# Kernel tuning notes

Measured on AMD Instinct MI355X. Metric: run time of the kernel, lower is better.

## Reference

```python
import math
import jax, jax.numpy as jnp
import numpy as np

B, T, C = 2, 2048, 1024
NH = 16
HS = C // NH
WIN = 256

def setup_inputs() -> dict:
    key = jax.random.key(0)
    k1, k2, k3 = jax.random.split(key, 3)
    x = jax.random.normal(k1, (B, T, C), dtype=jnp.float32)
    # Linear weights stored as (in, out) so y = x @ W
    scale_attn = 1.0 / math.sqrt(C)
    W_attn = jax.random.normal(k2, (C, 3 * C), dtype=jnp.float32) * scale_attn
    W_proj = jax.random.normal(k3, (C, C), dtype=jnp.float32) * scale_attn
    return {"x": x, "W_attn": W_attn, "W_proj": W_proj}

def reference(x, W_attn, W_proj):
    Bs, Ts, Cs = x.shape
    W = min(WIN, Ts)
    qkv = x @ W_attn                                  # [B,T,3C]
    q, k, v = jnp.split(qkv, 3, axis=-1)
    # [B,T,C] -> [B,NH,T,HS]
    q = q.reshape(Bs, Ts, NH, HS).transpose(0, 2, 1, 3)
    k = k.reshape(Bs, Ts, NH, HS).transpose(0, 2, 1, 3)
    v = v.reshape(Bs, Ts, NH, HS).transpose(0, 2, 1, 3)
    att = jnp.einsum('bhqd,bhkd->bhqk', q, k) * (1.0 / math.sqrt(HS))
    i_idx = jnp.arange(Ts)[:, None]
    j_idx = jnp.arange(Ts)[None, :]
    mask = (j_idx <= i_idx) & (i_idx - j_idx < W)      # causal sliding window
    att = jnp.where(mask[None, None, :, :], att, -jnp.inf)
    att = jax.nn.softmax(att, axis=-1)
    y = jnp.einsum('bhqk,bhkd->bhqd', att, v)          # [B,NH,T,HS]
    y = y.transpose(0, 2, 1, 3).reshape(Bs, Ts, Cs)
    return y @ W_proj
```

## Files before the change

kernel.cpp:

```cpp
#include <hip/hip_runtime.h>
#include <hip/hip_bf16.h>
#include <cstdint>

#define B_   2
#define T_   2048
#define C_   1024
#define NH_  16
#define HS_  64
#define WIN_ 256
#define M_   (B_*T_)

typedef __attribute__((ext_vector_type(8)))  short          short8;
typedef __attribute__((ext_vector_type(8)))  unsigned short ushortx8;
typedef __attribute__((ext_vector_type(8)))  __bf16         bf16x8;
typedef __attribute__((ext_vector_type(4)))  float          floatx4;
typedef __attribute__((ext_vector_type(16))) float          floatx16;

__device__ __forceinline__ unsigned short f2bf(float f) {
    union { float f; uint32_t u; } v; v.f = f;
    uint32_t r = (v.u + 0x7FFFu + ((v.u >> 16) & 1u)) >> 16;
    return (unsigned short)r;
}

__device__ __forceinline__ floatx4 mfma16(short8 a, short8 b, floatx4 c) {
    return __builtin_amdgcn_mfma_f32_16x16x32_bf16(
        __builtin_bit_cast(bf16x8, a), __builtin_bit_cast(bf16x8, b), c, 0, 0, 0);
}
__device__ __forceinline__ floatx16 mfma32(short8 a, short8 b, floatx16 c) {
    return __builtin_amdgcn_mfma_f32_32x32x16_bf16(
        __builtin_bit_cast(bf16x8, a), __builtin_bit_cast(bf16x8, b), c, 0, 0, 0);
}

__device__ __forceinline__ void async16(const void* g, void* l) {
    __builtin_amdgcn_global_load_lds(
        (const __attribute__((address_space(1))) void*)g,
        (__attribute__((address_space(3))) void*)l, 16, 0, 0);
}

#define NB_CONV 4096
#define NB_WA   768
#define NB_WP   256

__device__ void transpose_tile(const float* __restrict__ in, unsigned short* __restrict__ out,
                               int K, int N, int kt, int nt, unsigned short (*tile)[65])
{
    const int k0 = kt * 64, n0 = nt * 64;
    const int tr = threadIdx.x >> 4;
    const int tc = (threadIdx.x & 15) * 4;
    #pragma unroll
    for (int it = 0; it < 4; it++) {
        int row = tr + it * 16;
        float4 v = *(const float4*)&in[(size_t)(k0 + row) * N + n0 + tc];
        tile[row][tc + 0] = f2bf(v.x);
        tile[row][tc + 1] = f2bf(v.y);
        tile[row][tc + 2] = f2bf(v.z);
        tile[row][tc + 3] = f2bf(v.w);
    }
    __syncthreads();
    #pragma unroll
    for (int it = 0; it < 4; it++) {
        int nrow = tr + it * 16;
        ushort4 h;
        h.x = tile[tc + 0][nrow]; h.y = tile[tc + 1][nrow];
        h.z = tile[tc + 2][nrow]; h.w = tile[tc + 3][nrow];
        *(ushort4*)&out[(size_t)(n0 + nrow) * K + k0 + tc] = h;
    }
}

__global__ __launch_bounds__(256)
void prep_kernel(const float* __restrict__ x, const float* __restrict__ W_attn,
                 const float* __restrict__ W_proj,
                 unsigned short* __restrict__ xb, unsigned short* __restrict__ Wa_t,
                 unsigned short* __restrict__ Wp_t)
{
    __shared__ unsigned short tile[64][65];
    const int bid = blockIdx.x;
    if (bid < NB_CONV) {
        int i = (bid * 256 + threadIdx.x) * 4;
        float4 v = *(const float4*)&x[i];
        ushort4 h;
        h.x = f2bf(v.x); h.y = f2bf(v.y); h.z = f2bf(v.z); h.w = f2bf(v.w);
        *(ushort4*)&xb[i] = h;
    } else if (bid < NB_CONV + NB_WA) {
        int idx = bid - NB_CONV;
        transpose_tile(W_attn, Wa_t, C_, 3 * C_, idx / 48, idx % 48, tile);
    } else {
        int idx = bid - NB_CONV - NB_WA;
        transpose_tile(W_proj, Wp_t, C_, C_, idx / 16, idx % 16, tile);
    }
}

template<int MT, bool OUT_BF16, bool VSPLIT>
__global__ __launch_bounds__(256)
void gemm32(const unsigned short* __restrict__ A,
            const unsigned short* __restrict__ Bt,
            void* __restrict__ Cp, unsigned short* __restrict__ vt,
            int M, int N, int K)
{
    constexpr int BK = 64;
    constexpr int BM = 64 * MT;
    __shared__ unsigned short As[BM * BK];
    __shared__ unsigned short Bs[128 * BK];

    const int tid  = threadIdx.x;
    const int lane = tid & 63;
    const int wave = tid >> 6;
    const int l32  = lane & 31;
    const int hi   = lane >> 5;
    const int px   = l32 & 7;
    const int wm   = (wave & 1) * 32 * MT;
    const int wn   = (wave >> 1) * 64;
    const int m0   = blockIdx.y * BM;
    const int n0   = blockIdx.x * 128;

    const int ri = lane >> 3;
    const int pg = lane & 7;
    const int gg = pg ^ ri;

    floatx16 acc[MT][2];
    #pragma unroll
    for (int i = 0; i < MT; i++)
        #pragma unroll
        for (int j = 0; j < 2; j++) acc[i][j] = (floatx16)(0.f);

    const unsigned short* gA = &A[(size_t)(m0 + wave * 8 + ri) * K + gg * 8];
    const unsigned short* gB = &Bt[(size_t)(n0 + wave * 8 + ri) * K + gg * 8];
    unsigned short* lA = &As[(wave * 8) * BK];
    unsigned short* lB = &Bs[(wave * 8) * BK];

    for (int k0 = 0; k0 < K; k0 += BK) {
        #pragma unroll
        for (int s = 0; s < 2 * MT; s++)
            async16(gA + k0 + (size_t)s * 32 * K, lA + s * 32 * BK);
        #pragma unroll
        for (int s = 0; s < 4; s++)
            async16(gB + k0 + (size_t)s * 32 * K, lB + s * 32 * BK);
        __syncthreads();

        #pragma unroll
        for (int ks = 0; ks < 4; ks++) {
            short8 af[MT], bfr[2];
            #pragma unroll
            for (int i = 0; i < MT; i++) {
                int r = wm + i * 32 + l32;
                int p = (ks * 2 + hi) ^ px;
                af[i] = *(const short8*)(&As[r * BK + p * 8]);
            }
            #pragma unroll
            for (int j = 0; j < 2; j++) {
                int r = wn + j * 32 + l32;
                int p = (ks * 2 + hi) ^ px;
                bfr[j] = *(const short8*)(&Bs[r * BK + p * 8]);
            }
            #pragma unroll
            for (int i = 0; i < MT; i++)
                #pragma unroll
                for (int j = 0; j < 2; j++)
                    acc[i][j] = mfma32(af[i], bfr[j], acc[i][j]);
        }
        __syncthreads();
    }

    #pragma unroll
    for (int i = 0; i < MT; i++)
        #pragma unroll
        for (int j = 0; j < 2; j++) {
            const int col  = n0 + wn + j * 32 + l32;
            const int row0 = m0 + wm + i * 32 + 4 * hi;
            if (VSPLIT && col >= 2 * C_) {
                const int hd = col - 2 * C_;
                const int hh = hd >> 6, d = hd & 63;
                #pragma unroll
                for (int g = 0; g < 4; g++) {
                    int rowg = row0 + 8 * g;
                    int bb = rowg >> 11, t = rowg & (T_ - 1);
                    ushort4 h4;
                    h4.x = f2bf(acc[i][j][g * 4 + 0]);
                    h4.y = f2bf(acc[i][j][g * 4 + 1]);
                    h4.z = f2bf(acc[i][j][g * 4 + 2]);
                    h4.w = f2bf(acc[i][j][g * 4 + 3]);
                    *(ushort4*)&vt[((size_t)(bb * NH_ + hh) * 64 + d) * T_ + t] = h4;
                }
            } else {
                #pragma unroll
                for (int g = 0; g < 4; g++)
                    #pragma unroll
                    for (int rr = 0; rr < 4; rr++) {
                        int row = row0 + 8 * g + rr;
                        if (OUT_BF16)
                            ((unsigned short*)Cp)[(size_t)row * N + col] = f2bf(acc[i][j][g * 4 + rr]);
                        else
                            ((float*)Cp)[(size_t)row * N + col] = acc[i][j][g * 4 + rr];
                    }
            }
        }
}

__global__ __launch_bounds__(256)
void attn_kernel(const unsigned short* __restrict__ qkv,
                 const unsigned short* __restrict__ vt,
                 unsigned short* __restrict__ y)
{
    __shared__ unsigned short Ks[64 * 64];
    __shared__ unsigned short Vs[64 * 64];
    __shared__ unsigned short Ps[4][16 * 72];

    const int tid  = threadIdx.x;
    const int lane = tid & 63;
    const int wave = tid >> 6;
    const int l16  = lane & 15;
    const int quad = lane >> 4;
    const int sw   = l16 & 7;

    const int g  = blockIdx.x;
    const int yq = g >> 3;
    const int hb = (g & 7) + 8 * (yq >> 5);
    const int qt = yq & 31;
    const int h  = hb & 15;
    const int b  = hb >> 4;

    const int q0b = qt * 64;
    const int q0w = q0b + wave * 16;
    const size_t base = (size_t)b * T_;
    const int ROW  = 3 * C_;
    const int qoff = h * HS_;
    const int koff = C_ + h * HS_;
    const size_t vbase = ((size_t)(b * NH_ + h) * 64) * T_;
    unsigned short* Pstrip = Ps[wave];
    const float SC = 0.125f * 1.44269504f;

    const int ri = lane >> 3;
    const int gg = (lane & 7) ^ ri;

    short8 aq[2];
    #pragma unroll
    for (int ks = 0; ks < 2; ks++)
        aq[ks] = *(const short8*)&qkv[(base + q0w + l16) * ROW + qoff + ks * 32 + quad * 8];

    floatx4 O[4];
    #pragma unroll
    for (int j = 0; j < 4; j++) O[j] = (floatx4){0.f, 0.f, 0.f, 0.f};
    float psum[4] = {0.f, 0.f, 0.f, 0.f};

    int kb_lo = q0b - (WIN_ - 1);
    kb_lo = (kb_lo > 0 ? kb_lo : 0) & ~63;

    for (int kb = kb_lo; kb <= q0b; kb += 64) {
        __syncthreads();
        #pragma unroll
        for (int c = 0; c < 2; c++) {
            int row = wave * 16 + c * 8;
            async16(&qkv[(base + kb + row + ri) * ROW + koff + gg * 8],
                    &Ks[row * 64]);
            async16(&vt[vbase + (size_t)(row + ri) * T_ + kb + gg * 8],
                    &Vs[row * 64]);
        }
        __syncthreads();

        floatx4 s[4];
        #pragma unroll
        for (int nt = 0; nt < 4; nt++) s[nt] = (floatx4){0.f, 0.f, 0.f, 0.f};
        #pragma unroll
        for (int ks = 0; ks < 2; ks++)
            #pragma unroll
            for (int nt = 0; nt < 4; nt++) {
                short8 bk = *(const short8*)&Ks[(nt * 16 + l16) * 64
                                                + (((ks * 4 + quad) ^ sw) * 8)];
                s[nt] = mfma16(aq[ks], bk, s[nt]);
            }

        #pragma unroll
        for (int nt = 0; nt < 4; nt++)
            #pragma unroll
            for (int r = 0; r < 4; r++) {
                int dist = (q0w + quad * 4 + r) - (kb + nt * 16 + l16);
                float sv = ((unsigned)dist < (unsigned)WIN_) ? s[nt][r] * SC : -1e30f;
                float e = exp2f(sv);
                psum[r] += e;
                s[nt][r] = e;
            }

        #pragma unroll
        for (int nt = 0; nt < 4; nt++)
            #pragma unroll
            for (int r = 0; r < 4; r++)
                Pstrip[(quad * 4 + r) * 72 + nt * 16 + l16] = f2bf(s[nt][r]);

        #pragma unroll
        for (int ks = 0; ks < 2; ks++) {
            short8 ap = *(const short8*)&Pstrip[l16 * 72 + ks * 32 + quad * 8];
            #pragma unroll
            for (int jt = 0; jt < 4; jt++) {
                short8 bv = *(const short8*)&Vs[(jt * 16 + l16) * 64
                                                + (((ks * 4 + quad) ^ sw) * 8)];
                O[jt] = mfma16(ap, bv, O[jt]);
            }
        }
    }

    #pragma unroll
    for (int r = 0; r < 4; r++) {
        #pragma unroll
        for (int off = 8; off >= 1; off >>= 1)
            psum[r] += __shfl_xor(psum[r], off, 64);
    }

    #pragma unroll
    for (int jt = 0; jt < 4; jt++)
        #pragma unroll
        for (int r = 0; r < 4; r++)
            Pstrip[(quad * 4 + r) * 72 + jt * 16 + l16] = f2bf(O[jt][r] / psum[r]);
    #pragma unroll
    for (int it = 0; it < 2; it++) {
        int c = lane + 64 * it;
        int qr = c >> 3, dc = (c & 7) * 8;
        *(ushortx8*)&y[(base + q0w + qr) * C_ + qoff + dc] =
            *(const ushortx8*)&Pstrip[qr * 72 + dc];
    }
}

extern "C" void kernel_launch(void* const* d_in, const int* in_sizes, int n_in,
                              void* d_out, int out_size, void* d_ws, size_t ws_size,
                              hipStream_t stream)
{
    const float* x      = (const float*)d_in[0];
    const float* W_attn = (const float*)d_in[1];
    const float* W_proj = (const float*)d_in[2];
    float* out = (float*)d_out;

    unsigned short* xb   = (unsigned short*)d_ws;
    unsigned short* Wa_t = xb   + (size_t)M_ * C_;
    unsigned short* Wp_t = Wa_t + (size_t)3 * C_ * C_;
    unsigned short* qkv  = Wp_t + (size_t)C_ * C_;
    unsigned short* y    = qkv  + (size_t)M_ * 3 * C_;
    unsigned short* vtg  = y    + (size_t)M_ * C_;

    dim3 blk(256);
    prep_kernel<<<NB_CONV + NB_WA + NB_WP, blk, 0, stream>>>(x, W_attn, W_proj, xb, Wa_t, Wp_t);
    gemm32<2, true, true><<<dim3((3 * C_) / 128, M_ / 128), blk, 0, stream>>>(
        xb, Wa_t, qkv, vtg, M_, 3 * C_, C_);
    attn_kernel<<<(T_ / 64) * NH_ * B_, blk, 0, stream>>>(qkv, vtg, y);
    gemm32<1, false, false><<<dim3(C_ / 128, M_ / 64), blk, 0, stream>>>(
        y, Wp_t, out, nullptr, M_, C_, C_);
}
```

Measured before the change: 150.8 us.

## Use 256x256 double-buffered 512-thread GEMM tile for the QKV projection

Replaces the QKV projection GEMM with a dedicated 8-wave kernel. Each block computes a 256x256 output tile and double-buffers the A and B LDS tiles, so the next K-slice loads while the current one is multiplied. The aim is more operand reuse per global load and overlap of loads with MFMA work. The cost is about 128KB of LDS per block and only 192 blocks in the grid, which risks leaving CUs idle and capping occupancy at one block per CU. The output projection keeps a simplified fp32-output version of the old kernel.

```diff
diff --git a/kernel.cpp b/kernel.cpp
--- a/kernel.cpp
+++ b/kernel.cpp
@@ -90,17 +90,15 @@
     }
 }
 
-template<int MT, bool OUT_BF16, bool VSPLIT>
-__global__ __launch_bounds__(256)
-void gemm32(const unsigned short* __restrict__ A,
-            const unsigned short* __restrict__ Bt,
-            void* __restrict__ Cp, unsigned short* __restrict__ vt,
-            int M, int N, int K)
+__global__ __launch_bounds__(512, 2)
+void gemm256(const unsigned short* __restrict__ A,
+             const unsigned short* __restrict__ Bt,
+             unsigned short* __restrict__ Cq, unsigned short* __restrict__ vt,
+             int M, int N, int K)
 {
     constexpr int BK = 64;
-    constexpr int BM = 64 * MT;
-    __shared__ unsigned short As[BM * BK];
-    __shared__ unsigned short Bs[128 * BK];
+    __shared__ unsigned short As[2][256 * BK];
+    __shared__ unsigned short Bs[2][256 * BK];
 
     const int tid  = threadIdx.x;
     const int lane = tid & 63;
@@ -108,52 +106,53 @@
     const int l32  = lane & 31;
     const int hi   = lane >> 5;
     const int px   = l32 & 7;
-    const int wm   = (wave & 1) * 32 * MT;
+    const int wm   = (wave & 1) * 128;
     const int wn   = (wave >> 1) * 64;
-    const int m0   = blockIdx.y * BM;
-    const int n0   = blockIdx.x * 128;
+    const int m0   = blockIdx.y * 256;
+    const int n0   = blockIdx.x * 256;
 
     const int ri = lane >> 3;
     const int pg = lane & 7;
     const int gg = pg ^ ri;
 
-    floatx16 acc[MT][2];
-    #pragma unroll
-    for (int i = 0; i < MT; i++)
+    floatx16 acc[4][2];
+    #pragma unroll
+    for (int i = 0; i < 4; i++)
         #pragma unroll
         for (int j = 0; j < 2; j++) acc[i][j] = (floatx16)(0.f);
 
     const unsigned short* gA = &A[(size_t)(m0 + wave * 8 + ri) * K + gg * 8];
     const unsigned short* gB = &Bt[(size_t)(n0 + wave * 8 + ri) * K + gg * 8];
-    unsigned short* lA = &As[(wave * 8) * BK];
-    unsigned short* lB = &Bs[(wave * 8) * BK];
-
-    for (int k0 = 0; k0 < K; k0 += BK) {
-        #pragma unroll
-        for (int s = 0; s < 2 * MT; s++)
-            async16(gA + k0 + (size_t)s * 32 * K, lA + s * 32 * BK);
+
+    auto stage = [&](int buf, int k0) {
         #pragma unroll
         for (int s = 0; s < 4; s++)
-            async16(gB + k0 + (size_t)s * 32 * K, lB + s * 32 * BK);
-        __syncthreads();
+            async16(gA + k0 + (size_t)s * 64 * K, &As[buf][(wave * 8 + s * 64) * BK]);
+        #pragma unroll
+        for (int s = 0; s < 4; s++)
+            async16(gB + k0 + (size_t)s * 64 * K, &Bs[buf][(wave * 8 + s * 64) * BK]);
+    };
+
+    const int NT = K / BK;
+    stage(0, 0);
+    __syncthreads();
+
+    for (int kt = 0; kt < NT; kt++) {
+        const int cur = kt & 1;
+        if (kt + 1 < NT) stage(cur ^ 1, (kt + 1) * BK);
 
         #pragma unroll
         for (int ks = 0; ks < 4; ks++) {
-            short8 af[MT], bfr[2];
-            #pragma unroll
-            for (int i = 0; i < MT; i++) {
-                int r = wm + i * 32 + l32;
-                int p = (ks * 2 + hi) ^ px;
-                af[i] = *(const short8*)(&As[r * BK + p * 8]);
-            }
-            #pragma unroll
-            for (int j = 0; j < 2; j++) {
-                int r = wn + j * 32 + l32;
-                int p = (ks * 2 + hi) ^ px;
-                bfr[j] = *(const short8*)(&Bs[r * BK + p * 8]);
-            }
-            #pragma unroll
-            for (int i = 0; i < MT; i++)
+            const int p = ((ks * 2 + hi) ^ px) * 8;
+            short8 af[4], bfr[2];
+            #pragma unroll
+            for (int i = 0; i < 4; i++)
+                af[i] = *(const short8*)&As[cur][(wm + i * 32 + l32) * BK + p];
+            #pragma unroll
+            for (int j = 0; j < 2; j++)
+                bfr[j] = *(const short8*)&Bs[cur][(wn + j * 32 + l32) * BK + p];
+            #pragma unroll
+            for (int i = 0; i < 4; i++)
                 #pragma unroll
                 for (int j = 0; j < 2; j++)
                     acc[i][j] = mfma32(af[i], bfr[j], acc[i][j]);
@@ -162,12 +161,12 @@
     }
 
     #pragma unroll
-    for (int i = 0; i < MT; i++)
+    for (int i = 0; i < 4; i++)
         #pragma unroll
         for (int j = 0; j < 2; j++) {
             const int col  = n0 + wn + j * 32 + l32;
             const int row0 = m0 + wm + i * 32 + 4 * hi;
-            if (VSPLIT && col >= 2 * C_) {
+            if (col >= 2 * C_) {
                 const int hd = col - 2 * C_;
                 const int hh = hd >> 6, d = hd & 63;
                 #pragma unroll
@@ -187,12 +186,95 @@
                     #pragma unroll
                     for (int rr = 0; rr < 4; rr++) {
                         int row = row0 + 8 * g + rr;
-                        if (OUT_BF16)
-                            ((unsigned short*)Cp)[(size_t)row * N + col] = f2bf(acc[i][j][g * 4 + rr]);
-                        else
-                            ((float*)Cp)[(size_t)row * N + col] = acc[i][j][g * 4 + rr];
+                        Cq[(size_t)row * N + col] = f2bf(acc[i][j][g * 4 + rr]);
                     }
             }
+        }
+}
+
+template<int MT>
+__global__ __launch_bounds__(256)
+void gemm32(const unsigned short* __restrict__ A,
+            const unsigned short* __restrict__ Bt,
+            float* __restrict__ Cp, int M, int N, int K)
+{
+    constexpr int BK = 64;
+    constexpr int BM = 64 * MT;
+    __shared__ unsigned short As[BM * BK];
+    __shared__ unsigned short Bs[128 * BK];
+
+    const int tid  = threadIdx.x;
+    const int lane = tid & 63;
+    const int wave = tid >> 6;
+    const int l32  = lane & 31;
+    const int hi   = lane >> 5;
+    const int px   = l32 & 7;
+    const int wm   = (wave & 1) * 32 * MT;
+    const int wn   = (wave >> 1) * 64;
+    const int m0   = blockIdx.y * BM;
+    const int n0   = blockIdx.x * 128;
+
+    const int ri = lane >> 3;
+    const int pg = lane & 7;
+    const int gg = pg ^ ri;
+
+    floatx16 acc[MT][2];
+    #pragma unroll
+    for (int i = 0; i < MT; i++)
+        #pragma unroll
+        for (int j = 0; j < 2; j++) acc[i][j] = (floatx16)(0.f);
+
+    const unsigned short* gA = &A[(size_t)(m0 + wave * 8 + ri) * K + gg * 8];
+    const unsigned short* gB = &Bt[(size_t)(n0 + wave * 8 + ri) * K + gg * 8];
+    unsigned short* lA = &As[(wave * 8) * BK];
+    unsigned short* lB = &Bs[(wave * 8) * BK];
+
+    for (int k0 = 0; k0 < K; k0 += BK) {
+        #pragma unroll
+        for (int s = 0; s < 2 * MT; s++)
+            async16(gA + k0 + (size_t)s * 32 * K, lA + s * 32 * BK);
+        #pragma unroll
+        for (int s = 0; s < 4; s++)
+            async16(gB + k0 + (size_t)s * 32 * K, lB + s * 32 * BK);
+        __syncthreads();
+
+        #pragma unroll
+        for (int ks = 0; ks < 4; ks++) {
+            short8 af[MT], bfr[2];
+            #pragma unroll
+            for (int i = 0; i < MT; i++) {
+                int r = wm + i * 32 + l32;
+                int p = (ks * 2 + hi) ^ px;
+                af[i] = *(const short8*)(&As[r * BK + p * 8]);
+            }
+            #pragma unroll
+            for (int j = 0; j < 2; j++) {
+                int r = wn + j * 32 + l32;
+                int p = (ks * 2 + hi) ^ px;
+                bfr[j] = *(const short8*)(&Bs[r * BK + p * 8]);
+            }
+            #pragma unroll
+            for (int i = 0; i < MT; i++)
+                #pragma unroll
+                for (int j = 0; j < 2; j++)
+                    acc[i][j] = mfma32(af[i], bfr[j], acc[i][j]);
+        }
+        __syncthreads();
+    }
+
+    #pragma unroll
+    for (int i = 0; i < MT; i++)
+        #pragma unroll
+        for (int j = 0; j < 2; j++) {
+            const int col  = n0 + wn + j * 32 + l32;
+            const int row0 = m0 + wm + i * 32 + 4 * hi;
+            #pragma unroll
+            for (int g = 0; g < 4; g++)
+                #pragma unroll
+                for (int rr = 0; rr < 4; rr++) {
+                    int row = row0 + 8 * g + rr;
+                    Cp[(size_t)row * N + col] = acc[i][j][g * 4 + rr];
+                }
         }
 }
 
@@ -337,9 +419,9 @@
 
     dim3 blk(256);
     prep_kernel<<<NB_CONV + NB_WA + NB_WP, blk, 0, stream>>>(x, W_attn, W_proj, xb, Wa_t, Wp_t);
-    gemm32<2, true, true><<<dim3((3 * C_) / 128, M_ / 128), blk, 0, stream>>>(
+    gemm256<<<dim3((3 * C_) / 256, M_ / 256), dim3(512), 0, stream>>>(
         xb, Wa_t, qkv, vtg, M_, 3 * C_, C_);
     attn_kernel<<<(T_ / 64) * NH_ * B_, blk, 0, stream>>>(qkv, vtg, y);
-    gemm32<1, false, false><<<dim3(C_ / 128, M_ / 64), blk, 0, stream>>>(
-        y, Wp_t, out, nullptr, M_, C_, C_);
-}
+    gemm32<1><<<dim3(C_ / 128, M_ / 64), blk, 0, stream>>>(
+        y, Wp_t, out, M_, C_, C_);
+}
```

Measured after the change: 157.9 us. 1.05x slower.

## Double-buffer GEMM shared-memory tiles to overlap async loads with MFMA

Applied to the files above, without the earlier changes.

The GEMM kernel now keeps two shared-memory buffers for the A and B tiles. It issues the async global-to-LDS loads for the next K tile before computing on the current one, and waits with a partial vmcnt so that memory latency overlaps the matrix-core work. The output projection GEMM also switches from 64-row to 128-row tiles, giving fewer blocks and more reuse of each B tile. The cost is double the LDS per block, which may lower occupancy. The hand-written vmcnt(8) count is tied to the load count per stage for MT=2.

```diff
diff --git a/kernel.cpp b/kernel.cpp
--- a/kernel.cpp
+++ b/kernel.cpp
@@ -92,15 +92,15 @@
 
 template<int MT, bool OUT_BF16, bool VSPLIT>
 __global__ __launch_bounds__(256)
-void gemm32(const unsigned short* __restrict__ A,
-            const unsigned short* __restrict__ Bt,
-            void* __restrict__ Cp, unsigned short* __restrict__ vt,
-            int M, int N, int K)
+void gemm32db(const unsigned short* __restrict__ A,
+              const unsigned short* __restrict__ Bt,
+              void* __restrict__ Cp, unsigned short* __restrict__ vt,
+              int M, int N, int K)
 {
     constexpr int BK = 64;
     constexpr int BM = 64 * MT;
-    __shared__ unsigned short As[BM * BK];
-    __shared__ unsigned short Bs[128 * BK];
+    __shared__ unsigned short As[2][BM * BK];
+    __shared__ unsigned short Bs[2][128 * BK];
 
     const int tid  = threadIdx.x;
     const int lane = tid & 63;
@@ -125,40 +125,52 @@
 
     const unsigned short* gA = &A[(size_t)(m0 + wave * 8 + ri) * K + gg * 8];
     const unsigned short* gB = &Bt[(size_t)(n0 + wave * 8 + ri) * K + gg * 8];
-    unsigned short* lA = &As[(wave * 8) * BK];
-    unsigned short* lB = &Bs[(wave * 8) * BK];
-
-    for (int k0 = 0; k0 < K; k0 += BK) {
+
+    auto stage = [&](int buf, int k0) {
         #pragma unroll
         for (int s = 0; s < 2 * MT; s++)
-            async16(gA + k0 + (size_t)s * 32 * K, lA + s * 32 * BK);
+            async16(gA + k0 + (size_t)s * 32 * K, &As[buf][(wave * 8 + s * 32) * BK]);
         #pragma unroll
         for (int s = 0; s < 4; s++)
-            async16(gB + k0 + (size_t)s * 32 * K, lB + s * 32 * BK);
-        __syncthreads();
-
+            async16(gB + k0 + (size_t)s * 32 * K, &Bs[buf][(wave * 8 + s * 32) * BK]);
+    };
+
+    const int NT = K / BK;
+    stage(0, 0);
+    asm volatile("s_waitcnt vmcnt(0)" ::: "memory");
+    __builtin_amdgcn_s_barrier();
+
+    for (int t = 0; t < NT; t++) {
+        const int cur = t & 1;
+        if (t + 1 < NT) {
+            stage(cur ^ 1, (t + 1) * BK);
+            asm volatile("s_waitcnt vmcnt(8)" ::: "memory");
+        } else {
+            asm volatile("s_waitcnt vmcnt(0)" ::: "memory");
+        }
+        __builtin_amdgcn_s_barrier();
+        __builtin_amdgcn_sched_barrier(0);
+
+        const unsigned short* cA = As[cur];
+        const unsigned short* cB = Bs[cur];
         #pragma unroll
         for (int ks = 0; ks < 4; ks++) {
+            const int p = ((ks * 2 + hi) ^ px) * 8;
             short8 af[MT], bfr[2];
             #pragma unroll
-            for (int i = 0; i < MT; i++) {
-                int r = wm + i * 32 + l32;
-                int p = (ks * 2 + hi) ^ px;
-                af[i] = *(const short8*)(&As[r * BK + p * 8]);
-            }
-            #pragma unroll
-            for (int j = 0; j < 2; j++) {
-                int r = wn + j * 32 + l32;
-                int p = (ks * 2 + hi) ^ px;
-                bfr[j] = *(const short8*)(&Bs[r * BK + p * 8]);
-            }
+            for (int i = 0; i < MT; i++)
+                af[i] = *(const short8*)(&cA[(wm + i * 32 + l32) * BK + p]);
+            #pragma unroll
+            for (int j = 0; j < 2; j++)
+                bfr[j] = *(const short8*)(&cB[(wn + j * 32 + l32) * BK + p]);
             #pragma unroll
             for (int i = 0; i < MT; i++)
                 #pragma unroll
                 for (int j = 0; j < 2; j++)
                     acc[i][j] = mfma32(af[i], bfr[j], acc[i][j]);
         }
-        __syncthreads();
+        asm volatile("" ::: "memory");
+        __builtin_amdgcn_s_barrier();
     }
 
     #pragma unroll
@@ -337,9 +349,9 @@
 
     dim3 blk(256);
     prep_kernel<<<NB_CONV + NB_WA + NB_WP, blk, 0, stream>>>(x, W_attn, W_proj, xb, Wa_t, Wp_t);
-    gemm32<2, true, true><<<dim3((3 * C_) / 128, M_ / 128), blk, 0, stream>>>(
+    gemm32db<2, true, true><<<dim3((3 * C_) / 128, M_ / 128), blk, 0, stream>>>(
         xb, Wa_t, qkv, vtg, M_, 3 * C_, C_);
     attn_kernel<<<(T_ / 64) * NH_ * B_, blk, 0, stream>>>(qkv, vtg, y);
-    gemm32<1, false, false><<<dim3(C_ / 128, M_ / 64), blk, 0, stream>>>(
+    gemm32db<2, false, false><<<dim3(C_ / 128, M_ / 128), blk, 0, stream>>>(
         y, Wp_t, out, nullptr, M_, C_, C_);
 }
```

After: 162.7 us. 1.08x slower.
